# Kernel optimization log

Hardware: AMD Instinct MI355X
Metric: run time of the kernel (lower is better)

## Reference

```python
import jax, jax.numpy as jnp
import numpy as np

B, N, R = 4, 16, 64        # batch, permuted axis size, inner spatial size
M, S = N // 2, R * 2       # block count, block size


def _glorot(key, shape):
    fan_in, fan_out = shape[-2], shape[-1]
    lim = np.sqrt(6.0 / (fan_in + fan_out)).astype(np.float32)
    return jax.random.uniform(key, shape, jnp.float32, -lim, lim)


def setup_inputs() -> dict:
    key = jax.random.key(0)
    ks = jax.random.split(key, 10)
    inp = {
        "x": jax.random.normal(ks[0], (B, N, R, N, R, 2), jnp.float32),
        "perm_idx": jax.random.permutation(ks[1], N).astype(jnp.int32),
    }
    for i, name in enumerate(["hr1", "hi1", "hr2", "hi2", "hr3", "hi3", "hr4", "hi4"]):
        inp[name] = _glorot(ks[2 + i], (M, S, S))
    return inp


def _bilin(v, p_right, p_left):
    # v: (B, m, s, m, s). First contract the last s-axis against p_right's
    # block matmuls (block index = axis 3), then the axis-2 s-axis against
    # p_left's block matmuls (block index = axis 1).
    t = jnp.einsum('bmiaj,ajk->bmiak', v, p_right)
    return jnp.einsum('xbjci,bjk->xbkci', t, p_left)


def reference(x, perm_idx, hr1, hi1, hr2, hi2, hr3, hi3, hr4, hi4):
    m = x.shape[1] // 2
    s = x.shape[2] * 2
    n, r = m * 2, s // 2
    x = x.take(perm_idx, axis=1).take(perm_idx, axis=3)
    x = x.reshape((-1, m, s, m, s, 2))
    x_re, x_im = x[..., 0], x[..., 1]

    y_re = (_bilin(x_re, hr1, hr1) + _bilin(x_re, hi1, hi1)
            + _bilin(x_im, hi2, hr2) + _bilin(x_im, hr2, hi2))
    y_im = (_bilin(x_im, hr3, hr3) + _bilin(x_im, hi3, hi3)
            + _bilin(x_re, hi4, hr4) + _bilin(x_re, hr4, hi4))

    y = jnp.stack([y_re, y_im], axis=-1)
    return y.reshape((-1, n, r, n, r, 2))
```

## Files before the change

### kernel.cpp

```cpp
#include <hip/hip_runtime.h>
#include <hip/hip_bf16.h>
#include <stdint.h>

typedef __attribute__((ext_vector_type(8))) short bf16x8;
typedef __attribute__((ext_vector_type(4))) float f32x4;
typedef __attribute__((ext_vector_type(16))) float f32x16;

#define MFMA32(a, b, c) __builtin_amdgcn_mfma_f32_32x32x16_bf16((a), (b), (c), 0, 0, 0)

__device__ __forceinline__ unsigned short f2bf_rn(float f) {
    union { __bf16 b; unsigned short u; } v;
    v.b = (__bf16)f;
    return v.u;
}

__device__ __forceinline__ unsigned int pk2(float lo, float hi) {
    union { unsigned short s[2]; unsigned int u; } r;
    r.s[0] = f2bf_rn(lo); r.s[1] = f2bf_rn(hi);
    return r.u;
}

__device__ __forceinline__ void gload_lds16(const void* g, void* l) {
    __builtin_amdgcn_global_load_lds(
        (const __attribute__((address_space(1))) void*)g,
        (__attribute__((address_space(3))) void*)l, 16, 0, 0);
}

__global__ __launch_bounds__(256) void prep_h(
    const float* __restrict__ h0, const float* __restrict__ h1,
    const float* __restrict__ h2, const float* __restrict__ h3,
    const float* __restrict__ h4, const float* __restrict__ h5,
    const float* __restrict__ h6, const float* __restrict__ h7,
    unsigned short* __restrict__ ht)
{
    const float* hmap[8] = {h0, h1, h2, h3, h4, h5, h6, h7};
    const int wg = blockIdx.x;
    const float* src = hmap[wg >> 3] + (wg & 7) * 16384;
    unsigned short* dst = ht + wg * 16384;
    __shared__ unsigned short tile[128 * 129];
    const int t = threadIdx.x;
    #pragma unroll 4
    for (int i = 0; i < 64; ++i) {
        int idx = t + 256 * i, r = idx >> 7, k = idx & 127;
        tile[r * 129 + k] = f2bf_rn(src[idx]);
    }
    __syncthreads();
    #pragma unroll 4
    for (int i = 0; i < 64; ++i) {
        int idx = t + 256 * i, k = idx >> 7, r = idx & 127;
        dst[idx] = tile[r * 129 + k];
    }
}

__global__ __launch_bounds__(256) void prep_x(
    const float* __restrict__ x, const int* __restrict__ perm,
    unsigned short* __restrict__ xre, unsigned short* __restrict__ xim)
{
    const int id = blockIdx.x * 256 + threadIdx.x;
    const int b = id >> 18;
    const int row = (id >> 8) & 1023;
    const int col0 = (id & 255) * 4;
    const int n1 = perm[row >> 6], r1 = row & 63;
    const int n2 = perm[col0 >> 6], r2 = col0 & 63;
    const int src = (((b * 16 + n1) * 64 + r1) * 16 + n2) * 64 + r2;
    const float4* s = (const float4*)(x + src * 2);
    float4 v0 = s[0], v1 = s[1];
    ushort4 re, im;
    re.x = f2bf_rn(v0.x); re.y = f2bf_rn(v0.z); re.z = f2bf_rn(v1.x); re.w = f2bf_rn(v1.z);
    im.x = f2bf_rn(v0.y); im.y = f2bf_rn(v0.w); im.z = f2bf_rn(v1.y); im.w = f2bf_rn(v1.w);
    const int o = id * 4;
    *(ushort4*)(xre + o) = re;
    *(ushort4*)(xim + o) = im;
}

__global__ __launch_bounds__(512, 2) void bilin_main(
    const unsigned short* __restrict__ xre,
    const unsigned short* __restrict__ xim,
    const unsigned short* __restrict__ ht,
    float* __restrict__ out)
{
    const int wg = blockIdx.x;
    const int q = wg & 7, p = (wg >> 3) & 7, b = wg >> 6;
    const int tid = threadIdx.x;
    const int lane = tid & 63, wid = tid >> 6;
    const int wn = wid & 3, h = wid >> 2;
    const int l31 = lane & 31, hl = lane >> 5;

    __shared__ __align__(16) unsigned short smem[81920];
    unsigned short* xlds = smem;

    constexpr int cseq[8]  = {0, 1, 6, 7, 2, 3, 4, 5};
    constexpr int rperm[8] = {0, 1, 3, 2, 4, 5, 7, 6};

    f32x16 yre[4], yim[4];
    #pragma unroll
    for (int i = 0; i < 4; ++i) {
        #pragma unroll
        for (int e = 0; e < 16; ++e) { yre[i][e] = 0.f; yim[i][e] = 0.f; }
    }

    const int wubase = tid & ~63;
    auto stage_h = [&](unsigned short* dst, int blk) {
        const unsigned short* src = ht + blk * 16384;
        #pragma unroll
        for (int r = 0; r < 4; ++r) {
            const int idx = r * 512 + tid;
            const int row = idx >> 4, cin = idx & 15;
            gload_lds16(src + row * 128 + ((cin ^ (row & 15)) << 3),
                        dst + ((r * 512 + wubase) << 3));
        }
    };
    auto stage_x = [&](const unsigned short* xp) {
        const unsigned short* src = xp + (size_t)(b * 1024 + p * 128) * 1024 + q * 128;
        #pragma unroll
        for (int r = 0; r < 4; ++r) {
            const int idx = r * 512 + tid;
            const int row = idx >> 4, cin = idx & 15;
            gload_lds16(src + row * 1024 + ((cin ^ (row & 15)) << 3),
                        xlds + ((r * 512 + wubase) << 3));
        }
    };

    auto ldr = [&](const unsigned short* base, int row, int ch) -> bf16x8 {
        return *(const bf16x8*)(base + row * 128 + ((ch ^ (row & 15)) << 3));
    };

    stage_h(smem + 16384, rperm[0] * 8 + q);
    stage_h(smem + 49152, 0 * 8 + p);
    stage_x(xre);
    __syncthreads();

    #pragma unroll
    for (int cc = 0; cc < 8; ++cc) {
        const unsigned short* wb = smem + 16384 + (cc & 1) * 16384;
        const unsigned short* lb = smem + 49152 + (cc & 1) * 16384;

        if (cc < 7) {
            stage_h(smem + 16384 + ((cc + 1) & 1) * 16384,
                    rperm[cseq[cc + 1]] * 8 + q);
            stage_h(smem + 49152 + ((cc + 1) & 1) * 16384,
                    cseq[cc + 1] * 8 + p);
        }

        f32x16 u[2];
        #pragma unroll
        for (int e = 0; e < 16; ++e) { u[0][e] = 0.f; u[1][e] = 0.f; }
        #pragma unroll
        for (int ks = 0; ks < 8; ++ks) {
            bf16x8 wfr = ldr(wb, wn * 32 + l31, 2 * ks + hl);
            #pragma unroll
            for (int m2 = 0; m2 < 2; ++m2) {
                bf16x8 xfr = ldr(xlds, h * 64 + m2 * 32 + l31, 2 * ks + hl);
                u[m2] = MFMA32(xfr, wfr, u[m2]);
            }
        }

        if (cc == 3) {
            __syncthreads();
            stage_x(xim);
        }

        #pragma unroll
        for (int t = 0; t < 4; ++t) {
            const int f = t >> 1, qa = (t & 1) * 2, qb = qa + 1;
            unsigned int lo0 = pk2(u[f][4 * qa + 0], u[f][4 * qa + 1]);
            unsigned int lo1 = pk2(u[f][4 * qa + 2], u[f][4 * qa + 3]);
            unsigned int hi0 = pk2(u[f][4 * qb + 0], u[f][4 * qb + 1]);
            unsigned int hi1 = pk2(u[f][4 * qb + 2], u[f][4 * qb + 3]);
            unsigned int sxl0 = (unsigned int)__shfl_xor((int)lo0, 32);
            unsigned int sxl1 = (unsigned int)__shfl_xor((int)lo1, 32);
            unsigned int sxh0 = (unsigned int)__shfl_xor((int)hi0, 32);
            unsigned int sxh1 = (unsigned int)__shfl_xor((int)hi1, 32);
            union { unsigned int d[4]; bf16x8 v; } ufu;
            ufu.d[0] = hl ? sxh0 : lo0;
            ufu.d[1] = hl ? sxh1 : lo1;
            ufu.d[2] = hl ? hi0 : sxl0;
            ufu.d[3] = hl ? hi1 : sxl1;
            #pragma unroll
            for (int mt = 0; mt < 4; ++mt) {
                bf16x8 lfr = ldr(lb, mt * 32 + l31, 8 * h + 2 * t + hl);
                if ((cc & 3) < 2) yre[mt] = MFMA32(lfr, ufu.v, yre[mt]);
                else              yim[mt] = MFMA32(lfr, ufu.v, yim[mt]);
            }
        }

        __syncthreads();
    }

    float* red = (float*)smem + wn * 8192;
    if (h == 1) {
        #pragma unroll
        for (int mt = 0; mt < 4; ++mt)
            #pragma unroll
            for (int q4 = 0; q4 < 4; ++q4) {
                f32x4 vr, vi;
                #pragma unroll
                for (int jj = 0; jj < 4; ++jj) {
                    vr[jj] = yre[mt][4 * q4 + jj];
                    vi[jj] = yim[mt][4 * q4 + jj];
                }
                *(f32x4*)(red + ((0 * 4 + mt) * 4 + q4) * 256 + lane * 4) = vr;
                *(f32x4*)(red + ((1 * 4 + mt) * 4 + q4) * 256 + lane * 4) = vi;
            }
    }
    __syncthreads();
    if (h == 0) {
        float2* o2 = (float2*)out;
        #pragma unroll
        for (int mt = 0; mt < 4; ++mt)
            #pragma unroll
            for (int q4 = 0; q4 < 4; ++q4) {
                f32x4 pr = *(const f32x4*)(red + ((0 * 4 + mt) * 4 + q4) * 256 + lane * 4);
                f32x4 pi = *(const f32x4*)(red + ((1 * 4 + mt) * 4 + q4) * 256 + lane * 4);
                #pragma unroll
                for (int jj = 0; jj < 4; ++jj) {
                    const int j = 4 * q4 + jj;
                    const int row = mt * 32 + (j & 3) + 8 * (j >> 2) + 4 * hl;
                    float2 v;
                    v.x = yre[mt][j] + pr[jj];
                    v.y = yim[mt][j] + pi[jj];
                    o2[(size_t)(b * 1024 + p * 128 + row) * 1024
                       + q * 128 + wn * 32 + l31] = v;
                }
            }
    }
}

extern "C" void kernel_launch(void* const* d_in, const int* in_sizes, int n_in,
                              void* d_out, int out_size, void* d_ws, size_t ws_size,
                              hipStream_t stream) {
    const float* x  = (const float*)d_in[0];
    const int* perm = (const int*)d_in[1];
    unsigned short* ws = (unsigned short*)d_ws;
    unsigned short* htp = ws;
    unsigned short* xre = ws + 1u * 1024u * 1024u;
    unsigned short* xim = ws + 5u * 1024u * 1024u;

    hipLaunchKernelGGL(prep_h, dim3(64), dim3(256), 0, stream,
        (const float*)d_in[2], (const float*)d_in[3], (const float*)d_in[4],
        (const float*)d_in[5], (const float*)d_in[6], (const float*)d_in[7],
        (const float*)d_in[8], (const float*)d_in[9], htp);
    hipLaunchKernelGGL(prep_x, dim3(4096), dim3(256), 0, stream,
        x, perm, xre, xim);
    hipLaunchKernelGGL(bilin_main, dim3(256), dim3(512), 0, stream,
        xre, xim, htp, (float*)d_out);
}
```

Before: 46.75 us.

## Fuse permutation and bf16 conversion of x into the main bilinear kernel

Removes the separate prep_x kernel: the main kernel now gathers the permuted fp32 x tile directly from global memory, converts to bf16 and writes both real and imaginary parts into LDS once. This avoids writing and rereading the bf16 intermediate copies of x through global memory and one kernel launch. To free LDS for both x parts, the left-side H buffer becomes single-buffered with staging moved after extra barriers, which may expose load latency.

```diff
diff --git a/kernel.cpp b/kernel.cpp
--- a/kernel.cpp
+++ b/kernel.cpp
@@ -52,32 +52,9 @@
     }
 }
 
-__global__ __launch_bounds__(256) void prep_x(
+__global__ __launch_bounds__(512, 2) void bilin_main(
     const float* __restrict__ x, const int* __restrict__ perm,
-    unsigned short* __restrict__ xre, unsigned short* __restrict__ xim)
-{
-    const int id = blockIdx.x * 256 + threadIdx.x;
-    const int b = id >> 18;
-    const int row = (id >> 8) & 1023;
-    const int col0 = (id & 255) * 4;
-    const int n1 = perm[row >> 6], r1 = row & 63;
-    const int n2 = perm[col0 >> 6], r2 = col0 & 63;
-    const int src = (((b * 16 + n1) * 64 + r1) * 16 + n2) * 64 + r2;
-    const float4* s = (const float4*)(x + src * 2);
-    float4 v0 = s[0], v1 = s[1];
-    ushort4 re, im;
-    re.x = f2bf_rn(v0.x); re.y = f2bf_rn(v0.z); re.z = f2bf_rn(v1.x); re.w = f2bf_rn(v1.z);
-    im.x = f2bf_rn(v0.y); im.y = f2bf_rn(v0.w); im.z = f2bf_rn(v1.y); im.w = f2bf_rn(v1.w);
-    const int o = id * 4;
-    *(ushort4*)(xre + o) = re;
-    *(ushort4*)(xim + o) = im;
-}
-
-__global__ __launch_bounds__(512, 2) void bilin_main(
-    const unsigned short* __restrict__ xre,
-    const unsigned short* __restrict__ xim,
-    const unsigned short* __restrict__ ht,
-    float* __restrict__ out)
+    const unsigned short* __restrict__ ht, float* __restrict__ out)
 {
     const int wg = blockIdx.x;
     const int q = wg & 7, p = (wg >> 3) & 7, b = wg >> 6;
@@ -87,17 +64,12 @@
     const int l31 = lane & 31, hl = lane >> 5;
 
     __shared__ __align__(16) unsigned short smem[81920];
-    unsigned short* xlds = smem;
+    unsigned short* xre_lds = smem;
+    unsigned short* xim_lds = smem + 16384;
+    unsigned short* llds = smem + 65536;
 
     constexpr int cseq[8]  = {0, 1, 6, 7, 2, 3, 4, 5};
     constexpr int rperm[8] = {0, 1, 3, 2, 4, 5, 7, 6};
-
-    f32x16 yre[4], yim[4];
-    #pragma unroll
-    for (int i = 0; i < 4; ++i) {
-        #pragma unroll
-        for (int e = 0; e < 16; ++e) { yre[i][e] = 0.f; yim[i][e] = 0.f; }
-    }
 
     const int wubase = tid & ~63;
     auto stage_h = [&](unsigned short* dst, int blk) {
@@ -110,37 +82,55 @@
                         dst + ((r * 512 + wubase) << 3));
         }
     };
-    auto stage_x = [&](const unsigned short* xp) {
-        const unsigned short* src = xp + (size_t)(b * 1024 + p * 128) * 1024 + q * 128;
-        #pragma unroll
-        for (int r = 0; r < 4; ++r) {
-            const int idx = r * 512 + tid;
-            const int row = idx >> 4, cin = idx & 15;
-            gload_lds16(src + row * 1024 + ((cin ^ (row & 15)) << 3),
-                        xlds + ((r * 512 + wubase) << 3));
-        }
-    };
 
     auto ldr = [&](const unsigned short* base, int row, int ch) -> bf16x8 {
         return *(const bf16x8*)(base + row * 128 + ((ch ^ (row & 15)) << 3));
     };
 
-    stage_h(smem + 16384, rperm[0] * 8 + q);
-    stage_h(smem + 49152, 0 * 8 + p);
-    stage_x(xre);
+    float4 xv[4][4];
+    int woffs[4];
+    #pragma unroll
+    for (int i = 0; i < 4; ++i) {
+        const int idx = i * 512 + tid;
+        const int row = idx >> 4, cin = idx & 15;
+        const int n1 = perm[2 * p + (row >> 6)];
+        const int n2 = perm[2 * q + (cin >> 3)];
+        const int r1 = row & 63, r2 = (cin & 7) * 8;
+        const float* sp = x + ((size_t)((b * 16 + n1) * 64 + r1) * 1024
+                               + n2 * 64 + r2) * 2;
+        #pragma unroll
+        for (int j = 0; j < 4; ++j)
+            xv[i][j] = *(const float4*)(sp + j * 4);
+        woffs[i] = row * 128 + ((cin ^ (row & 15)) << 3);
+    }
+    stage_h(smem + 32768, rperm[0] * 8 + q);
+    stage_h(llds, 0 * 8 + p);
+    #pragma unroll
+    for (int i = 0; i < 4; ++i) {
+        bf16x8 re, im;
+        #pragma unroll
+        for (int j = 0; j < 4; ++j) {
+            re[2 * j]     = (short)f2bf_rn(xv[i][j].x);
+            re[2 * j + 1] = (short)f2bf_rn(xv[i][j].z);
+            im[2 * j]     = (short)f2bf_rn(xv[i][j].y);
+            im[2 * j + 1] = (short)f2bf_rn(xv[i][j].w);
+        }
+        *(bf16x8*)(xre_lds + woffs[i]) = re;
+        *(bf16x8*)(xim_lds + woffs[i]) = im;
+    }
     __syncthreads();
 
+    f32x16 yre[4], yim[4];
+    #pragma unroll
+    for (int i = 0; i < 4; ++i) {
+        #pragma unroll
+        for (int e = 0; e < 16; ++e) { yre[i][e] = 0.f; yim[i][e] = 0.f; }
+    }
+
     #pragma unroll
     for (int cc = 0; cc < 8; ++cc) {
-        const unsigned short* wb = smem + 16384 + (cc & 1) * 16384;
-        const unsigned short* lb = smem + 49152 + (cc & 1) * 16384;
-
-        if (cc < 7) {
-            stage_h(smem + 16384 + ((cc + 1) & 1) * 16384,
-                    rperm[cseq[cc + 1]] * 8 + q);
-            stage_h(smem + 49152 + ((cc + 1) & 1) * 16384,
-                    cseq[cc + 1] * 8 + p);
-        }
+        const unsigned short* wb = smem + 32768 + (cc & 1) * 16384;
+        const unsigned short* xg = (cc < 4) ? xre_lds : xim_lds;
 
         f32x16 u[2];
         #pragma unroll
@@ -150,15 +140,15 @@
             bf16x8 wfr = ldr(wb, wn * 32 + l31, 2 * ks + hl);
             #pragma unroll
             for (int m2 = 0; m2 < 2; ++m2) {
-                bf16x8 xfr = ldr(xlds, h * 64 + m2 * 32 + l31, 2 * ks + hl);
+                bf16x8 xfr = ldr(xg, h * 64 + m2 * 32 + l31, 2 * ks + hl);
                 u[m2] = MFMA32(xfr, wfr, u[m2]);
             }
         }
 
-        if (cc == 3) {
-            __syncthreads();
-            stage_x(xim);
-        }
+        __syncthreads();
+        if (cc < 7)
+            stage_h(smem + 32768 + ((cc + 1) & 1) * 16384,
+                    rperm[cseq[cc + 1]] * 8 + q);
 
         #pragma unroll
         for (int t = 0; t < 4; ++t) {
@@ -178,13 +168,15 @@
             ufu.d[3] = hl ? hi1 : sxl1;
             #pragma unroll
             for (int mt = 0; mt < 4; ++mt) {
-                bf16x8 lfr = ldr(lb, mt * 32 + l31, 8 * h + 2 * t + hl);
+                bf16x8 lfr = ldr(llds, mt * 32 + l31, 8 * h + 2 * t + hl);
                 if ((cc & 3) < 2) yre[mt] = MFMA32(lfr, ufu.v, yre[mt]);
                 else              yim[mt] = MFMA32(lfr, ufu.v, yim[mt]);
             }
         }
 
         __syncthreads();
+        if (cc < 7)
+            stage_h(llds, cseq[cc + 1] * 8 + p);
     }
 
     float* red = (float*)smem + wn * 8192;
@@ -231,17 +223,12 @@
                               hipStream_t stream) {
     const float* x  = (const float*)d_in[0];
     const int* perm = (const int*)d_in[1];
-    unsigned short* ws = (unsigned short*)d_ws;
-    unsigned short* htp = ws;
-    unsigned short* xre = ws + 1u * 1024u * 1024u;
-    unsigned short* xim = ws + 5u * 1024u * 1024u;
+    unsigned short* htp = (unsigned short*)d_ws;
 
     hipLaunchKernelGGL(prep_h, dim3(64), dim3(256), 0, stream,
         (const float*)d_in[2], (const float*)d_in[3], (const float*)d_in[4],
         (const float*)d_in[5], (const float*)d_in[6], (const float*)d_in[7],
         (const float*)d_in[8], (const float*)d_in[9], htp);
-    hipLaunchKernelGGL(prep_x, dim3(4096), dim3(256), 0, stream,
-        x, perm, xre, xim);
     hipLaunchKernelGGL(bilin_main, dim3(256), dim3(512), 0, stream,
-        xre, xim, htp, (float*)d_out);
-}
+        x, perm, htp, (float*)d_out);
+}
```

Result: faster. 42.48 us (-9.1%).
